# Optimization experiments

Hardware: AMD Instinct MI355X
Metric: run time of the kernel (lower is better)

The kernel has to match this reference:

```python
import jax, jax.numpy as jnp
import numpy as np

N_NODES = 100000
N_EDGES = 800000
EPS = 1e-5


def _mean_agg(h, src, dst):
    # DGL SAGEConv 'mean': average of in-neighbor features per dst node.
    msg = jnp.take(h, src, axis=0)                      # [E, D] gather
    summed = jax.ops.segment_sum(msg, dst, num_segments=N_NODES)
    deg = jax.ops.segment_sum(jnp.ones((src.shape[0],), h.dtype), dst,
                              num_segments=N_NODES)
    return summed / jnp.maximum(deg, 1.0)[:, None]


def _sage(h, src, dst, ws, wn, b):
    # rst = fc_self(h) + fc_neigh(mean_neigh) + bias
    return h @ ws + _mean_agg(h, src, dst) @ wn + b


def _bn(x, g, b, m, v):
    return (x - m) * (g / jnp.sqrt(v + EPS)) + b


def setup_inputs() -> dict:
    key = jax.random.key(0)
    ks = jax.random.split(key, 16)
    s = 0.02
    inp = {
        "structural_features": jax.random.normal(ks[0], (N_NODES, 128), jnp.float32),
        "multimodal_features": jax.random.normal(ks[1], (N_NODES, 384), jnp.float32),
        "src": jax.random.randint(ks[2], (N_EDGES,), 0, N_NODES),
        "dst": jax.random.randint(ks[3], (N_EDGES,), 0, N_NODES),
        "enc_w": jax.random.normal(ks[4], (512, 128), jnp.float32) * s,
        "enc_b": jnp.zeros((128,), jnp.float32),
        "sage0_ws": jax.random.normal(ks[5], (128, 256), jnp.float32) * s,
        "sage0_wn": jax.random.normal(ks[6], (128, 256), jnp.float32) * s,
        "sage0_b": jnp.zeros((256,), jnp.float32),
        "bn0_g": jnp.ones((256,), jnp.float32),
        "bn0_b": jnp.zeros((256,), jnp.float32),
        "bn0_m": jnp.zeros((256,), jnp.float32),
        "bn0_v": jnp.ones((256,), jnp.float32),
        "sage1_ws": jax.random.normal(ks[7], (256, 128), jnp.float32) * s,
        "sage1_wn": jax.random.normal(ks[8], (256, 128), jnp.float32) * s,
        "sage1_b": jnp.zeros((128,), jnp.float32),
        "bn1_g": jnp.ones((128,), jnp.float32),
        "bn1_b": jnp.zeros((128,), jnp.float32),
        "bn1_m": jnp.zeros((128,), jnp.float32),
        "bn1_v": jnp.ones((128,), jnp.float32),
        "rel_w": jax.random.normal(ks[9], (256, 128), jnp.float32) * s,
        "rel_b": jnp.zeros((128,), jnp.float32),
        "cls_w1": jax.random.normal(ks[10], (128, 64), jnp.float32) * s,
        "cls_b1": jnp.zeros((64,), jnp.float32),
        "cls_w2": jax.random.normal(ks[11], (64, 32), jnp.float32) * s,
        "cls_b2": jnp.zeros((32,), jnp.float32),
    }
    return inp


def reference(structural_features, multimodal_features, src, dst,
              enc_w, enc_b,
              sage0_ws, sage0_wn, sage0_b, bn0_g, bn0_b, bn0_m, bn0_v,
              sage1_ws, sage1_wn, sage1_b, bn1_g, bn1_b, bn1_m, bn1_v,
              rel_w, rel_b, cls_w1, cls_b1, cls_w2, cls_b2):
    x = jnp.concatenate([structural_features, multimodal_features], axis=-1)
    h0 = jax.nn.relu(x @ enc_w + enc_b)                     # input_encoder (dropout=eval)
    h = jax.nn.relu(_bn(_sage(h0, src, dst, sage0_ws, sage0_wn, sage0_b),
                        bn0_g, bn0_b, bn0_m, bn0_v))
    h = jax.nn.relu(_bn(_sage(h, src, dst, sage1_ws, sage1_wn, sage1_b),
                        bn1_g, bn1_b, bn1_m, bn1_v))
    h_final = jnp.concatenate([h0, h], axis=1)              # [N, 256]
    h_final = jax.nn.relu(h_final @ rel_w + rel_b)          # relation_encoder
    out = jax.nn.relu(h_final @ cls_w1 + cls_b1) @ cls_w2 + cls_b2
    return out
```

## Files before the change

### kernel.cpp

```cpp
#include <hip/hip_runtime.h>
#include <math.h>


#define EPS 1e-5f

typedef __attribute__((ext_vector_type(8))) short bf16x8;
typedef __attribute__((ext_vector_type(4))) float f32x4;

__device__ inline unsigned short f2bf(float x) {
    unsigned u = __float_as_uint(x);
    u += 0x7fff + ((u >> 16) & 1);
    return (unsigned short)(u >> 16);
}
__device__ inline float bf2f(unsigned short h) {
    return __uint_as_float(((unsigned)h) << 16);
}
__device__ inline unsigned packbf(float x, float y) {
    return (unsigned)f2bf(x) | ((unsigned)f2bf(y) << 16);
}

__device__ inline void gload_lds16(const void* g, void* l) {
    __builtin_amdgcn_global_load_lds(
        (__attribute__((address_space(1))) void*)g,
        (__attribute__((address_space(3))) void*)l, 16, 0, 0);
}


__global__ void count_deg(const int* __restrict__ dst, int* __restrict__ deg, int e) {
    int i = blockIdx.x * 256 + threadIdx.x;
    if (i < e) atomicAdd(&deg[dst[i]], 1);
}

__global__ __launch_bounds__(1024)
void scan_block(const int* __restrict__ deg, int* __restrict__ rowptr,
                int* __restrict__ part, int n) {
    __shared__ int buf[1024];
    const int tid = threadIdx.x;
    const int i = blockIdx.x * 1024 + tid;
    const int v = (i < n) ? deg[i] : 0;
    buf[tid] = v;
    __syncthreads();
    #pragma unroll 1
    for (int off = 1; off < 1024; off <<= 1) {
        int t = (tid >= off) ? buf[tid - off] : 0;
        __syncthreads();
        buf[tid] += t;
        __syncthreads();
    }
    if (i < n) rowptr[i] = buf[tid] - v;
    if (tid == 1023) part[blockIdx.x] = buf[1023];
}

__global__ __launch_bounds__(1024)
void scan_part(int* __restrict__ part, int nb) {
    __shared__ int buf[1024];
    const int tid = threadIdx.x;
    const int v = (tid < nb) ? part[tid] : 0;
    buf[tid] = v;
    __syncthreads();
    #pragma unroll 1
    for (int off = 1; off < 1024; off <<= 1) {
        int t = (tid >= off) ? buf[tid - off] : 0;
        __syncthreads();
        buf[tid] += t;
        __syncthreads();
    }
    if (tid < nb) part[tid] = buf[tid] - v;
    if (tid == 1023) part[nb] = buf[1023];
}

__global__ void scan_add(const int* __restrict__ part, int* __restrict__ rowptr,
                         int* __restrict__ cursor, int n, int nb) {
    int i = blockIdx.x * 256 + threadIdx.x;
    if (i < n) {
        int v = rowptr[i] + part[i >> 10];
        rowptr[i] = v;
        cursor[i] = v;
    }
    if (i == 0) rowptr[n] = part[nb];
}

__global__ void fill_edges(const int* __restrict__ src, const int* __restrict__ dst,
                           int* __restrict__ cursor, int* __restrict__ eidx, int e) {
    int i = blockIdx.x * 256 + threadIdx.x;
    if (i < e) {
        int pos = atomicAdd(&cursor[dst[i]], 1);
        eidx[pos] = src[i];
    }
}


__global__ __launch_bounds__(256)
void prep_all(const float* __restrict__ enc_w, const float* __restrict__ s0_ws,
              const float* __restrict__ s0_wn, const float* __restrict__ s1_ws,
              const float* __restrict__ s1_wn, const float* __restrict__ rel_w,
              const float* __restrict__ cw1, const float* __restrict__ cw2,
              short* wt_enc_h, short* wt_enc_l, short* wt_s0_h, short* wt_s0_l,
              short* wt_st_h, short* wt_st_l, short* wt_rel_h, short* wt_rel_l,
              short* wt_c1_h, short* wt_c1_l, short* wt_c2_h, short* wt_c2_l) {
    int e = blockIdx.x * 256 + threadIdx.x;
    const float* W; short* hi; short* lo; int Nd, ldt, koff;
    if (e < 65536)       { W = enc_w; hi = wt_enc_h; lo = wt_enc_l; Nd = 128; ldt = 512; koff = 0; }
    else if (e < 98304)  { e -= 65536;  W = s0_ws; hi = wt_s0_h; lo = wt_s0_l; Nd = 256; ldt = 256; koff = 0; }
    else if (e < 131072) { e -= 98304;  W = s0_wn; hi = wt_s0_h; lo = wt_s0_l; Nd = 256; ldt = 256; koff = 128; }
    else if (e < 163840) { e -= 131072; W = s1_ws; hi = wt_st_h; lo = wt_st_l; Nd = 128; ldt = 256; koff = 0; }
    else if (e < 196608) { e -= 163840; W = s1_wn; hi = wt_st_h + 32768; lo = wt_st_l + 32768; Nd = 128; ldt = 256; koff = 0; }
    else if (e < 229376) { e -= 196608; W = rel_w; hi = wt_rel_h; lo = wt_rel_l; Nd = 128; ldt = 256; koff = 0; }
    else if (e < 237568) { e -= 229376; W = cw1; hi = wt_c1_h; lo = wt_c1_l; Nd = 64; ldt = 128; koff = 0; }
    else if (e < 239616) { e -= 237568; W = cw2; hi = wt_c2_h; lo = wt_c2_l; Nd = 32; ldt = 64; koff = 0; }
    else return;
    const int k = e / Nd, n = e - k * Nd;
    const float x = W[e];
    const unsigned short h = f2bf(x);
    const unsigned short l = f2bf(x - bf2f(h));
    const size_t o = (size_t)n * ldt + koff + k;
    hi[o] = (short)h;
    lo[o] = (short)l;
}


__global__ __launch_bounds__(256)
void agg_mean_bb(const short* __restrict__ featb,
                 const int* __restrict__ rowptr, const int* __restrict__ eidx,
                 short* __restrict__ outb, int n) {
    const int node = blockIdx.x * 4 + (threadIdx.x >> 6);
    if (node >= n) return;
    const int lane = threadIdx.x & 63;
    const int g = lane >> 4, j = lane & 15;
    const int beg = rowptr[node], end = rowptr[node + 1];
    float s[8];
    #pragma unroll
    for (int i = 0; i < 8; ++i) s[i] = 0.f;
    for (int e = beg + g; e < end; e += 8) {
        const int e1 = e + 4;
        const bool has2 = e1 < end;
        const int i0 = eidx[e];
        const int i1 = has2 ? eidx[e1] : i0;
        const uint4 v0 = *(const uint4*)(featb + (size_t)i0 * 128 + j * 8);
        const uint4 v1 = *(const uint4*)(featb + (size_t)i1 * 128 + j * 8);
        __builtin_amdgcn_sched_barrier(0);
        s[0] += __uint_as_float(v0.x << 16); s[1] += __uint_as_float(v0.x & 0xffff0000u);
        s[2] += __uint_as_float(v0.y << 16); s[3] += __uint_as_float(v0.y & 0xffff0000u);
        s[4] += __uint_as_float(v0.z << 16); s[5] += __uint_as_float(v0.z & 0xffff0000u);
        s[6] += __uint_as_float(v0.w << 16); s[7] += __uint_as_float(v0.w & 0xffff0000u);
        if (has2) {
            s[0] += __uint_as_float(v1.x << 16); s[1] += __uint_as_float(v1.x & 0xffff0000u);
            s[2] += __uint_as_float(v1.y << 16); s[3] += __uint_as_float(v1.y & 0xffff0000u);
            s[4] += __uint_as_float(v1.z << 16); s[5] += __uint_as_float(v1.z & 0xffff0000u);
            s[6] += __uint_as_float(v1.w << 16); s[7] += __uint_as_float(v1.w & 0xffff0000u);
        }
    }
    #pragma unroll
    for (int i = 0; i < 8; ++i) {
        s[i] += __shfl_xor(s[i], 32);
        s[i] += __shfl_xor(s[i], 16);
    }
    if (g == 0) {
        const float inv = 1.0f / fmaxf((float)(end - beg), 1.0f);
        uint4 o;
        o.x = packbf(s[0] * inv, s[1] * inv);
        o.y = packbf(s[2] * inv, s[3] * inv);
        o.z = packbf(s[4] * inv, s[5] * inv);
        o.w = packbf(s[6] * inv, s[7] * inv);
        *(uint4*)(outb + (size_t)node * 128 + j * 8) = o;
    }
}

__global__ __launch_bounds__(256)
void agg_combine_bb(const short* __restrict__ featb,
                    const int* __restrict__ rowptr, const int* __restrict__ eidx,
                    const float* __restrict__ s1,
                    const float* __restrict__ bias,
                    const float* __restrict__ bng, const float* __restrict__ bnb,
                    const float* __restrict__ bnm, const float* __restrict__ bnv,
                    short* __restrict__ outb, int n) {
    const int node = blockIdx.x * 4 + (threadIdx.x >> 6);
    if (node >= n) return;
    const int lane = threadIdx.x & 63;
    const int g = lane >> 4, j = lane & 15;
    const int beg = rowptr[node], end = rowptr[node + 1];
    float s[8];
    #pragma unroll
    for (int i = 0; i < 8; ++i) s[i] = 0.f;
    for (int e = beg + g; e < end; e += 8) {
        const int e1 = e + 4;
        const bool has2 = e1 < end;
        const int i0 = eidx[e];
        const int i1 = has2 ? eidx[e1] : i0;
        const uint4 v0 = *(const uint4*)(featb + (size_t)i0 * 128 + j * 8);
        const uint4 v1 = *(const uint4*)(featb + (size_t)i1 * 128 + j * 8);
        __builtin_amdgcn_sched_barrier(0);
        s[0] += __uint_as_float(v0.x << 16); s[1] += __uint_as_float(v0.x & 0xffff0000u);
        s[2] += __uint_as_float(v0.y << 16); s[3] += __uint_as_float(v0.y & 0xffff0000u);
        s[4] += __uint_as_float(v0.z << 16); s[5] += __uint_as_float(v0.z & 0xffff0000u);
        s[6] += __uint_as_float(v0.w << 16); s[7] += __uint_as_float(v0.w & 0xffff0000u);
        if (has2) {
            s[0] += __uint_as_float(v1.x << 16); s[1] += __uint_as_float(v1.x & 0xffff0000u);
            s[2] += __uint_as_float(v1.y << 16); s[3] += __uint_as_float(v1.y & 0xffff0000u);
            s[4] += __uint_as_float(v1.z << 16); s[5] += __uint_as_float(v1.z & 0xffff0000u);
            s[6] += __uint_as_float(v1.w << 16); s[7] += __uint_as_float(v1.w & 0xffff0000u);
        }
    }
    #pragma unroll
    for (int i = 0; i < 8; ++i) {
        s[i] += __shfl_xor(s[i], 32);
        s[i] += __shfl_xor(s[i], 16);
    }
    if (g == 0) {
        const float inv = 1.0f / fmaxf((float)(end - beg), 1.0f);
        const int c0 = j * 8;
        const float4 a0 = *(const float4*)(s1 + (size_t)node * 128 + c0);
        const float4 a1 = *(const float4*)(s1 + (size_t)node * 128 + c0 + 4);
        const float sf[8] = {a0.x, a0.y, a0.z, a0.w, a1.x, a1.y, a1.z, a1.w};
        float r[8];
        #pragma unroll
        for (int i = 0; i < 8; ++i) {
            const int c = c0 + i;
            float v = sf[i] + s[i] * inv + bias[c];
            v = (v - bnm[c]) * (bng[c] / sqrtf(bnv[c] + EPS)) + bnb[c];
            r[i] = fmaxf(v, 0.f);
        }
        uint4 o;
        o.x = packbf(r[0], r[1]); o.y = packbf(r[2], r[3]);
        o.z = packbf(r[4], r[5]); o.w = packbf(r[6], r[7]);
        *(uint4*)(outb + (size_t)node * 128 + j * 8) = o;
    }
}

template<int NT, int K1, int K2>
__global__ __launch_bounds__(256)
void gemm_dp(const short* __restrict__ A1, int lda1,
             const short* __restrict__ A2, int lda2,
             const short* __restrict__ Wt_hi, const short* __restrict__ Wt_lo,
             const float* __restrict__ bias,
             const float* __restrict__ bng, const float* __restrict__ bnb,
             const float* __restrict__ bnm, const float* __restrict__ bnv,
             int relu,
             float* __restrict__ Cf, int fpN, int ldc,
             short* __restrict__ Cb, int bfcol0, int ldcb,
             int M) {
    constexpr int K   = K1 + K2;
    constexpr int NBK = K / 64;
    constexpr int NTW = NT / 2;
    static_assert(K % 64 == 0, "K multiple of 64");
    static_assert(NT % 2 == 0, "NT even");
    static_assert(K2 == 0 || K1 % 64 == 0, "concat boundary on BK");
    constexpr int ASZ = 128 * 64;
    constexpr int BSZ = 2 * NT * 16 * 64;
    constexpr int BUF = ASZ + BSZ;
    __shared__ short lds[2 * BUF];

    const int tid  = threadIdx.x;
    const int lane = tid & 63;
    const int wv   = tid >> 6;
    const int wm   = wv >> 1;
    const int wn   = wv & 1;
    const int bm   = blockIdx.y * 128;
    const int col0 = blockIdx.x * (NT * 16);
    const int lrow = lane & 15;
    const int quad = lane >> 4;

    const int su = (tid & 7) ^ ((tid >> 3) & 7);
    const short* gsA1[4];
    const short* gsA2[4];
    #pragma unroll
    for (int jj = 0; jj < 4; ++jj) {
        const int rg = min(bm + jj * 32 + (tid >> 3), M - 1);
        gsA1[jj] = A1 + (size_t)rg * lda1 + su * 8;
        if constexpr (K2 > 0) gsA2[jj] = A2 + (size_t)rg * lda2 + su * 8;
        else gsA2[jj] = nullptr;
    }
    const short* gsB[NT];
    #pragma unroll
    for (int jj = 0; jj < NT; ++jj) {
        const int colIdx = jj * 32 + (tid >> 3);
        const bool ishi = colIdx < NT * 16;
        const int cp = ishi ? colIdx : colIdx - NT * 16;
        gsB[jj] = (ishi ? Wt_hi : Wt_lo) + (size_t)(col0 + cp) * K + su * 8;
    }

    auto stage = [&](int b, int c) {
        const int k = c * 64;
        #pragma unroll
        for (int jj = 0; jj < 4; ++jj) {
            const short* p;
            if constexpr (K2 > 0)
                p = (k < K1) ? (gsA1[jj] + k) : (gsA2[jj] + (k - K1));
            else
                p = gsA1[jj] + k;
            gload_lds16(p, &lds[b * BUF + (jj * 256 + tid) * 8]);
        }
        #pragma unroll
        for (int jj = 0; jj < NT; ++jj)
            gload_lds16(gsB[jj] + k, &lds[b * BUF + ASZ + (jj * 256 + tid) * 8]);
    };

    int aoff[4][2];
    #pragma unroll
    for (int m = 0; m < 4; ++m)
        #pragma unroll
        for (int kk = 0; kk < 2; ++kk)
            aoff[m][kk] = (wm * 64 + m * 16 + lrow) * 64 +
                          (((kk * 4 + quad) ^ (lrow & 7)) * 8);
    int boff[NTW][2];
    #pragma unroll
    for (int nt = 0; nt < NTW; ++nt)
        #pragma unroll
        for (int kk = 0; kk < 2; ++kk)
            boff[nt][kk] = (wn * NTW * 16 + nt * 16 + lrow) * 64 +
                           (((kk * 4 + quad) ^ (lrow & 7)) * 8);

    f32x4 acc[4][NTW];
    #pragma unroll
    for (int m = 0; m < 4; ++m)
        #pragma unroll
        for (int nt = 0; nt < NTW; ++nt)
            acc[m][nt] = (f32x4){0.f, 0.f, 0.f, 0.f};

    stage(0, 0);

    for (int c = 0; c < NBK; ++c) {
        const int b = c & 1;
        if (c + 1 < NBK) {
            stage(b ^ 1, c + 1);
            if constexpr (NT == 4) asm volatile("s_waitcnt vmcnt(8)" ::: "memory");
            else                   asm volatile("s_waitcnt vmcnt(6)" ::: "memory");
        } else {
            asm volatile("s_waitcnt vmcnt(0)" ::: "memory");
        }
        __builtin_amdgcn_s_barrier();

        const short* La = &lds[b * BUF];
        const short* Lb = &lds[b * BUF + ASZ];
        #pragma unroll
        for (int kk = 0; kk < 2; ++kk) {
            bf16x8 a[4];
            #pragma unroll
            for (int m = 0; m < 4; ++m)
                a[m] = *(const bf16x8*)(La + aoff[m][kk]);
            #pragma unroll
            for (int nt = 0; nt < NTW; ++nt) {
                const bf16x8 vbh = *(const bf16x8*)(Lb + boff[nt][kk]);
                const bf16x8 vbl = *(const bf16x8*)(Lb + boff[nt][kk] + NT * 16 * 64);
                #pragma unroll
                for (int m = 0; m < 4; ++m) {
                    acc[m][nt] = __builtin_amdgcn_mfma_f32_16x16x32_bf16(a[m], vbh, acc[m][nt], 0, 0, 0);
                    acc[m][nt] = __builtin_amdgcn_mfma_f32_16x16x32_bf16(a[m], vbl, acc[m][nt], 0, 0, 0);
                }
            }
        }
        asm volatile("" ::: "memory");
        __builtin_amdgcn_s_barrier();
    }

    constexpr int EW = NT * 16 + 4;
    float* ep = (float*)lds;

    #pragma unroll
    for (int nt = 0; nt < NTW; ++nt) {
        const int lcol = wn * NTW * 16 + nt * 16 + lrow;
        const int gcol = col0 + lcol;
        const float bsc = bias ? bias[gcol] : 0.f;
        float gg = 1.f, bb = 0.f, mm = 0.f;
        if (bng) { gg = bng[gcol] / sqrtf(bnv[gcol] + EPS); bb = bnb[gcol]; mm = bnm[gcol]; }
        #pragma unroll
        for (int m = 0; m < 4; ++m) {
            #pragma unroll
            for (int r = 0; r < 4; ++r) {
                float x = acc[m][nt][r] + bsc;
                if (bng) x = (x - mm) * gg + bb;
                if (relu) x = fmaxf(x, 0.f);
                ep[(wm * 64 + m * 16 + quad * 4 + r) * EW + lcol] = x;
            }
        }
    }
    __syncthreads();

    if (col0 < fpN) {
        for (int g = tid; g < 128 * NT * 4; g += 256) {
            const int row = g / (NT * 4), u = g - row * (NT * 4);
            const int grow = bm + row;
            if (grow < M)
                *(float4*)(Cf + (size_t)grow * ldc + col0 + u * 4) =
                    *(const float4*)(ep + row * EW + u * 4);
        }
    } else {
        for (int g = tid; g < 128 * NT * 2; g += 256) {
            const int row = g / (NT * 2), u = g - row * (NT * 2);
            const int grow = bm + row;
            const float4 f0 = *(const float4*)(ep + row * EW + u * 8);
            const float4 f1 = *(const float4*)(ep + row * EW + u * 8 + 4);
            uint4 o;
            o.x = packbf(f0.x, f0.y); o.y = packbf(f0.z, f0.w);
            o.z = packbf(f1.x, f1.y); o.w = packbf(f1.z, f1.w);
            if (grow < M)
                *(uint4*)(Cb + (size_t)grow * ldcb + (col0 - bfcol0) + u * 8) = o;
        }
    }
}

__global__ __launch_bounds__(256)
void gemm_enc(const float* __restrict__ A1f,
              const float* __restrict__ A2f,
              const short* __restrict__ Wt_hi, const short* __restrict__ Wt_lo,
              const float* __restrict__ bias,
              short* __restrict__ Cb, int ldcb, int M) {
    constexpr int NT = 4, NTW = 2, K = 512, NBK = 8;
    constexpr int ASZ = 128 * 64;
    constexpr int BSZ = 2 * NT * 16 * 64;
    constexpr int BUF = ASZ + BSZ;
    __shared__ short lds[2 * BUF];

    const int tid  = threadIdx.x;
    const int lane = tid & 63;
    const int wv   = tid >> 6;
    const int wm   = wv >> 1;
    const int wn   = wv & 1;
    const int bm   = blockIdx.y * 128;
    const int col0 = blockIdx.x * (NT * 16);
    const int lrow = lane & 15;
    const int quad = lane >> 4;

    const int su = (tid & 7) ^ ((tid >> 3) & 7);
    const float* gsA1[4];
    const float* gsA2[4];
    #pragma unroll
    for (int jj = 0; jj < 4; ++jj) {
        const int rg = min(bm + jj * 32 + (tid >> 3), M - 1);
        gsA1[jj] = A1f + (size_t)rg * 128 + su * 8;
        gsA2[jj] = A2f + (size_t)rg * 384 + su * 8;
    }
    const short* gsB[NT];
    #pragma unroll
    for (int jj = 0; jj < NT; ++jj) {
        const int colIdx = jj * 32 + (tid >> 3);
        const bool ishi = colIdx < NT * 16;
        const int cp = ishi ? colIdx : colIdx - NT * 16;
        gsB[jj] = (ishi ? Wt_hi : Wt_lo) + (size_t)(col0 + cp) * K + su * 8;
    }
    auto stageB = [&](int b, int c) {
        const int k = c * 64;
        #pragma unroll
        for (int jj = 0; jj < NT; ++jj)
            gload_lds16(gsB[jj] + k, &lds[b * BUF + ASZ + (jj * 256 + tid) * 8]);
    };

    int aoff[4][2], boff[NTW][2];
    #pragma unroll
    for (int m = 0; m < 4; ++m)
        #pragma unroll
        for (int kk = 0; kk < 2; ++kk)
            aoff[m][kk] = (wm * 64 + m * 16 + lrow) * 64 +
                          (((kk * 4 + quad) ^ (lrow & 7)) * 8);
    #pragma unroll
    for (int nt = 0; nt < NTW; ++nt)
        #pragma unroll
        for (int kk = 0; kk < 2; ++kk)
            boff[nt][kk] = (wn * NTW * 16 + nt * 16 + lrow) * 64 +
                           (((kk * 4 + quad) ^ (lrow & 7)) * 8);

    f32x4 acc[4][NTW];
    #pragma unroll
    for (int m = 0; m < 4; ++m)
        #pragma unroll
        for (int nt = 0; nt < NTW; ++nt)
            acc[m][nt] = (f32x4){0.f, 0.f, 0.f, 0.f};

    float4 awin[8];

    #pragma unroll
    for (int jj = 0; jj < 4; ++jj) {
        awin[jj * 2 + 0] = *(const float4*)(gsA1[jj]);
        awin[jj * 2 + 1] = *(const float4*)(gsA1[jj] + 4);
    }
    stageB(0, 0);
    #pragma unroll
    for (int jj = 0; jj < 4; ++jj) {
        const float4 w0 = awin[jj * 2 + 0], w1 = awin[jj * 2 + 1];
        uint4 o;
        o.x = packbf(w0.x, w0.y); o.y = packbf(w0.z, w0.w);
        o.z = packbf(w1.x, w1.y); o.w = packbf(w1.z, w1.w);
        *((uint4*)&lds[(jj * 256 + tid) * 8]) = o;
    }
    asm volatile("s_waitcnt vmcnt(0)" ::: "memory");
    __builtin_amdgcn_s_barrier();

    #pragma unroll
    for (int c = 0; c < NBK; ++c) {
        const int cur = c & 1, nxt = cur ^ 1;
        if (c + 1 < NBK) {
            const int k1 = (c + 1) * 64;
            #pragma unroll
            for (int jj = 0; jj < 4; ++jj) {
                const float* p = (k1 < 128) ? (gsA1[jj] + k1)
                                            : (gsA2[jj] + (k1 - 128));
                awin[jj * 2 + 0] = *(const float4*)p;
                awin[jj * 2 + 1] = *(const float4*)(p + 4);
            }
            stageB(nxt, c + 1);
            __builtin_amdgcn_sched_barrier(0);
        }

        const short* La = &lds[cur * BUF];
        const short* Lb = &lds[cur * BUF + ASZ];
        #pragma unroll
        for (int kk = 0; kk < 2; ++kk) {
            bf16x8 a[4];
            #pragma unroll
            for (int m = 0; m < 4; ++m)
                a[m] = *(const bf16x8*)(La + aoff[m][kk]);
            #pragma unroll
            for (int nt = 0; nt < NTW; ++nt) {
                const bf16x8 vbh = *(const bf16x8*)(Lb + boff[nt][kk]);
                const bf16x8 vbl = *(const bf16x8*)(Lb + boff[nt][kk] + NT * 16 * 64);
                #pragma unroll
                for (int m = 0; m < 4; ++m) {
                    acc[m][nt] = __builtin_amdgcn_mfma_f32_16x16x32_bf16(a[m], vbh, acc[m][nt], 0, 0, 0);
                    acc[m][nt] = __builtin_amdgcn_mfma_f32_16x16x32_bf16(a[m], vbl, acc[m][nt], 0, 0, 0);
                }
            }
        }

        if (c + 1 < NBK) {
            #pragma unroll
            for (int jj = 0; jj < 4; ++jj) {
                const float4 w0 = awin[jj * 2 + 0], w1 = awin[jj * 2 + 1];
                uint4 o;
                o.x = packbf(w0.x, w0.y); o.y = packbf(w0.z, w0.w);
                o.z = packbf(w1.x, w1.y); o.w = packbf(w1.z, w1.w);
                *((uint4*)&lds[nxt * BUF + (jj * 256 + tid) * 8]) = o;
            }
            asm volatile("s_waitcnt vmcnt(0)" ::: "memory");
            __builtin_amdgcn_s_barrier();
        }
    }
    __builtin_amdgcn_s_barrier();

    constexpr int EW = NT * 16 + 4;
    float* ep = (float*)lds;
    #pragma unroll
    for (int nt = 0; nt < NTW; ++nt) {
        const int lcol = wn * NTW * 16 + nt * 16 + lrow;
        const float bsc = bias[col0 + lcol];
        #pragma unroll
        for (int m = 0; m < 4; ++m)
            #pragma unroll
            for (int r = 0; r < 4; ++r)
                ep[(wm * 64 + m * 16 + quad * 4 + r) * EW + lcol] =
                    fmaxf(acc[m][nt][r] + bsc, 0.f);
    }
    __syncthreads();
    for (int g = tid; g < 128 * NT * 2; g += 256) {
        const int row = g / (NT * 2), u = g - row * (NT * 2);
        const int grow = bm + row;
        const float4 f0 = *(const float4*)(ep + row * EW + u * 8);
        const float4 f1 = *(const float4*)(ep + row * EW + u * 8 + 4);
        uint4 o;
        o.x = packbf(f0.x, f0.y); o.y = packbf(f0.z, f0.w);
        o.z = packbf(f1.x, f1.y); o.w = packbf(f1.z, f1.w);
        if (grow < M)
            *(uint4*)(Cb + (size_t)grow * ldcb + col0 + u * 8) = o;
    }
}

__global__ __launch_bounds__(256)
void gemm_cls(const short* __restrict__ A1,
              const short* __restrict__ W1h, const short* __restrict__ W1l,
              const float* __restrict__ cb1,
              const short* __restrict__ W2h, const short* __restrict__ W2l,
              const float* __restrict__ cb2,
              float* __restrict__ out, int M) {
    constexpr int NT = 4, NTW = 2, NBK = 2, K = 128;
    constexpr int ASZ = 128 * 64, BSZ = 2 * NT * 16 * 64, BUF = ASZ + BSZ;
    __shared__ short lds[2 * BUF];

    const int tid  = threadIdx.x;
    const int lane = tid & 63;
    const int wv   = tid >> 6;
    const int wm   = wv >> 1;
    const int wn   = wv & 1;
    const int bm   = blockIdx.x * 128;
    const int lrow = lane & 15;
    const int quad = lane >> 4;

    const int su = (tid & 7) ^ ((tid >> 3) & 7);
    const short* gsA[4];
    #pragma unroll
    for (int jj = 0; jj < 4; ++jj) {
        const int rg = min(bm + jj * 32 + (tid >> 3), M - 1);
        gsA[jj] = A1 + (size_t)rg * 128 + su * 8;
    }
    const short* gsB[NT];
    #pragma unroll
    for (int jj = 0; jj < NT; ++jj) {
        const int colIdx = jj * 32 + (tid >> 3);
        const bool ishi = colIdx < NT * 16;
        const int cp = ishi ? colIdx : colIdx - NT * 16;
        gsB[jj] = (ishi ? W1h : W1l) + (size_t)cp * K + su * 8;
    }
    auto stage = [&](int b, int c) {
        const int k = c * 64;
        #pragma unroll
        for (int jj = 0; jj < 4; ++jj)
            gload_lds16(gsA[jj] + k, &lds[b * BUF + (jj * 256 + tid) * 8]);
        #pragma unroll
        for (int jj = 0; jj < NT; ++jj)
            gload_lds16(gsB[jj] + k, &lds[b * BUF + ASZ + (jj * 256 + tid) * 8]);
    };

    int aoff[4][2], boff[NTW][2];
    #pragma unroll
    for (int m = 0; m < 4; ++m)
        #pragma unroll
        for (int kk = 0; kk < 2; ++kk)
            aoff[m][kk] = (wm * 64 + m * 16 + lrow) * 64 +
                          (((kk * 4 + quad) ^ (lrow & 7)) * 8);
    #pragma unroll
    for (int nt = 0; nt < NTW; ++nt)
        #pragma unroll
        for (int kk = 0; kk < 2; ++kk)
            boff[nt][kk] = (wn * NTW * 16 + nt * 16 + lrow) * 64 +
                           (((kk * 4 + quad) ^ (lrow & 7)) * 8);

    f32x4 acc[4][NTW];
    #pragma unroll
    for (int m = 0; m < 4; ++m)
        #pragma unroll
        for (int nt = 0; nt < NTW; ++nt)
            acc[m][nt] = (f32x4){0.f, 0.f, 0.f, 0.f};

    stage(0, 0);
    for (int c = 0; c < NBK; ++c) {
        const int b = c & 1;
        if (c + 1 < NBK) {
            stage(b ^ 1, c + 1);
            asm volatile("s_waitcnt vmcnt(8)" ::: "memory");
        } else {
            asm volatile("s_waitcnt vmcnt(0)" ::: "memory");
        }
        __builtin_amdgcn_s_barrier();
        const short* La = &lds[b * BUF];
        const short* Lb = &lds[b * BUF + ASZ];
        #pragma unroll
        for (int kk = 0; kk < 2; ++kk) {
            bf16x8 a[4];
            #pragma unroll
            for (int m = 0; m < 4; ++m)
                a[m] = *(const bf16x8*)(La + aoff[m][kk]);
            #pragma unroll
            for (int nt = 0; nt < NTW; ++nt) {
                const bf16x8 vbh = *(const bf16x8*)(Lb + boff[nt][kk]);
                const bf16x8 vbl = *(const bf16x8*)(Lb + boff[nt][kk] + NT * 16 * 64);
                #pragma unroll
                for (int m = 0; m < 4; ++m) {
                    acc[m][nt] = __builtin_amdgcn_mfma_f32_16x16x32_bf16(a[m], vbh, acc[m][nt], 0, 0, 0);
                    acc[m][nt] = __builtin_amdgcn_mfma_f32_16x16x32_bf16(a[m], vbl, acc[m][nt], 0, 0, 0);
                }
            }
        }
        asm volatile("" ::: "memory");
        __builtin_amdgcn_s_barrier();
    }

    constexpr int EW = 68;
    float* ep = (float*)lds;
    #pragma unroll
    for (int nt = 0; nt < NTW; ++nt) {
        const int lcol = wn * NTW * 16 + nt * 16 + lrow;
        const float bsc = cb1[lcol];
        #pragma unroll
        for (int m = 0; m < 4; ++m)
            #pragma unroll
            for (int r = 0; r < 4; ++r)
                ep[(wm * 64 + m * 16 + quad * 4 + r) * EW + lcol] =
                    fmaxf(acc[m][nt][r] + bsc, 0.f);
    }
    __syncthreads();

    const short* pB2h = W2h + (size_t)(wn * 16 + lrow) * 64 + quad * 8;
    const short* pB2l = W2l + (size_t)(wn * 16 + lrow) * 64 + quad * 8;
    f32x4 acc2[4];
    #pragma unroll
    for (int m = 0; m < 4; ++m) acc2[m] = (f32x4){0.f, 0.f, 0.f, 0.f};
    #pragma unroll
    for (int kk = 0; kk < 2; ++kk) {
        const bf16x8 bh = *(const bf16x8*)(pB2h + kk * 32);
        const bf16x8 bl = *(const bf16x8*)(pB2l + kk * 32);
        #pragma unroll
        for (int m = 0; m < 4; ++m) {
            const float* pe = ep + (wm * 64 + m * 16 + lrow) * EW + kk * 32 + quad * 8;
            const float4 e0 = *(const float4*)pe;
            const float4 e1 = *(const float4*)(pe + 4);
            bf16x8 a;
            a[0] = (short)f2bf(e0.x); a[1] = (short)f2bf(e0.y);
            a[2] = (short)f2bf(e0.z); a[3] = (short)f2bf(e0.w);
            a[4] = (short)f2bf(e1.x); a[5] = (short)f2bf(e1.y);
            a[6] = (short)f2bf(e1.z); a[7] = (short)f2bf(e1.w);
            acc2[m] = __builtin_amdgcn_mfma_f32_16x16x32_bf16(a, bh, acc2[m], 0, 0, 0);
            acc2[m] = __builtin_amdgcn_mfma_f32_16x16x32_bf16(a, bl, acc2[m], 0, 0, 0);
        }
    }

    constexpr int EW2 = 36;
    float* ep2 = (float*)lds + 128 * EW;
    {
        const int lcol = wn * 16 + lrow;
        const float bsc = cb2[lcol];
        #pragma unroll
        for (int m = 0; m < 4; ++m)
            #pragma unroll
            for (int r = 0; r < 4; ++r)
                ep2[(wm * 64 + m * 16 + quad * 4 + r) * EW2 + lcol] =
                    acc2[m][r] + bsc;
    }
    __syncthreads();
    #pragma unroll
    for (int j = 0; j < 4; ++j) {
        const int g = tid + j * 256;
        const int row = g >> 3, u = g & 7;
        const int grow = bm + row;
        if (grow < M)
            *(float4*)(out + (size_t)grow * 32 + u * 4) =
                *(const float4*)(ep2 + row * EW2 + u * 4);
    }
}


extern "C" void kernel_launch(void* const* d_in, const int* in_sizes, int n_in,
                              void* d_out, int out_size, void* d_ws, size_t ws_size,
                              hipStream_t stream) {
    const float* sf    = (const float*)d_in[0];
    const float* mf    = (const float*)d_in[1];
    const int*   src   = (const int*)d_in[2];
    const int*   dst   = (const int*)d_in[3];
    const float* enc_w = (const float*)d_in[4];
    const float* enc_b = (const float*)d_in[5];
    const float* s0_ws = (const float*)d_in[6];
    const float* s0_wn = (const float*)d_in[7];
    const float* s0_b  = (const float*)d_in[8];
    const float* bn0_g = (const float*)d_in[9];
    const float* bn0_b = (const float*)d_in[10];
    const float* bn0_m = (const float*)d_in[11];
    const float* bn0_v = (const float*)d_in[12];
    const float* s1_ws = (const float*)d_in[13];
    const float* s1_wn = (const float*)d_in[14];
    const float* s1_b  = (const float*)d_in[15];
    const float* bn1_g = (const float*)d_in[16];
    const float* bn1_b = (const float*)d_in[17];
    const float* bn1_m = (const float*)d_in[18];
    const float* bn1_v = (const float*)d_in[19];
    const float* rel_w = (const float*)d_in[20];
    const float* rel_b = (const float*)d_in[21];
    const float* cw1   = (const float*)d_in[22];
    const float* cb1   = (const float*)d_in[23];
    const float* cw2   = (const float*)d_in[24];
    const float* cb2   = (const float*)d_in[25];
    float* out = (float*)d_out;

    const int nn = in_sizes[0] / 128;
    const int ne = in_sizes[2];
    const int nb = (nn + 1023) / 1024;

    short* h0b   = (short*)d_ws;
    short* xb    = h0b + (size_t)nn * 128;
    float* st    = (float*)xb;
    short* h1b   = (short*)(st + (size_t)nn * 128);
    short* agg0b = xb + (size_t)nn * 512;
    short* t1b   = agg0b + (size_t)nn * 128;
    short* h2b   = t1b + (size_t)nn * 128;
    short* rb    = t1b;
    int* deg    = (int*)(h2b + (size_t)nn * 128);
    int* rowptr = deg + nn;
    int* cursor = rowptr + nn + 1;
    int* part   = cursor + nn;
    int* eidx   = part + nb + 1;
    short* wts = (short*)(eidx + ne);
    short* wt_enc_h = wts;                 short* wt_enc_l = wt_enc_h + 65536;
    short* wt_s0_h  = wt_enc_l + 65536;    short* wt_s0_l  = wt_s0_h  + 65536;
    short* wt_st_h  = wt_s0_l  + 65536;    short* wt_st_l  = wt_st_h  + 65536;
    short* wt_rel_h = wt_st_l  + 65536;    short* wt_rel_l = wt_rel_h + 32768;
    short* wt_c1_h  = wt_rel_l + 32768;    short* wt_c1_l  = wt_c1_h  + 8192;
    short* wt_c2_h  = wt_c1_l  + 8192;     short* wt_c2_l  = wt_c2_h  + 2048;

    const dim3 blk(256);
    const int gM = (nn + 127) / 128;

    hipMemsetAsync(deg, 0, (size_t)nn * 4, stream);
    count_deg <<<dim3((ne + 255) / 256), blk, 0, stream>>>(dst, deg, ne);
    scan_block<<<dim3(nb), dim3(1024), 0, stream>>>(deg, rowptr, part, nn);
    scan_part <<<dim3(1),  dim3(1024), 0, stream>>>(part, nb);
    scan_add  <<<dim3((nn + 255) / 256), blk, 0, stream>>>(part, rowptr, cursor, nn, nb);
    fill_edges<<<dim3((ne + 255) / 256), blk, 0, stream>>>(src, dst, cursor, eidx, ne);

    prep_all<<<dim3(936), blk, 0, stream>>>(
        enc_w, s0_ws, s0_wn, s1_ws, s1_wn, rel_w, cw1, cw2,
        wt_enc_h, wt_enc_l, wt_s0_h, wt_s0_l, wt_st_h, wt_st_l,
        wt_rel_h, wt_rel_l, wt_c1_h, wt_c1_l, wt_c2_h, wt_c2_l);

    gemm_enc<<<dim3(2, gM), blk, 0, stream>>>(
        sf, mf, wt_enc_h, wt_enc_l, enc_b, h0b, 128, nn);

    agg_mean_bb<<<dim3((nn + 3) / 4), blk, 0, stream>>>(
        h0b, rowptr, eidx, agg0b, nn);

    gemm_dp<4, 128, 128><<<dim3(4, gM), blk, 0, stream>>>(
        h0b, 128, agg0b, 128, wt_s0_h, wt_s0_l, s0_b,
        bn0_g, bn0_b, bn0_m, bn0_v, 1,
        nullptr, 0, 0, h1b, 0, 256, nn);

    gemm_dp<4, 256, 0><<<dim3(4, gM), blk, 0, stream>>>(
        h1b, 256, nullptr, 0, wt_st_h, wt_st_l, nullptr,
        nullptr, nullptr, nullptr, nullptr, 0,
        st, 128, 128, t1b, 128, 128, nn);

    agg_combine_bb<<<dim3((nn + 3) / 4), blk, 0, stream>>>(
        t1b, rowptr, eidx, st, s1_b,
        bn1_g, bn1_b, bn1_m, bn1_v, h2b, nn);

    gemm_dp<4, 128, 128><<<dim3(2, gM), blk, 0, stream>>>(
        h0b, 128, h2b, 128, wt_rel_h, wt_rel_l, rel_b,
        nullptr, nullptr, nullptr, nullptr, 1,
        nullptr, 0, 0, rb, 0, 128, nn);

    gemm_cls<<<dim3(gM), blk, 0, stream>>>(
        rb, wt_c1_h, wt_c1_l, cb1, wt_c2_h, wt_c2_l, cb2, out, nn);
}
```

Before: 661.3 us.

## Fuse relation encoder GEMM into classifier kernel to skip intermediate round trip

Merges the relation-encoder GEMM (concat of h0 and h2, K=256, N=128) with the two classifier layers into a single kernel. Each block now computes the full 128-column relation output and keeps it in LDS as the input to cls layer 1, with cls weights read straight from global memory. This removes one launch and the bf16 write and re-read of the intermediate relation tensor. In exchange, grid parallelism drops from 2*gM to gM blocks and each block's register and LDS footprint grows, which may lower occupancy.

```diff
diff --git a/kernel.cpp b/kernel.cpp
--- a/kernel.cpp
+++ b/kernel.cpp
@@ -564,14 +564,19 @@
 }
 
 __global__ __launch_bounds__(256)
-void gemm_cls(const short* __restrict__ A1,
-              const short* __restrict__ W1h, const short* __restrict__ W1l,
-              const float* __restrict__ cb1,
-              const short* __restrict__ W2h, const short* __restrict__ W2l,
-              const float* __restrict__ cb2,
-              float* __restrict__ out, int M) {
-    constexpr int NT = 4, NTW = 2, NBK = 2, K = 128;
-    constexpr int ASZ = 128 * 64, BSZ = 2 * NT * 16 * 64, BUF = ASZ + BSZ;
+void gemm_relcls(const short* __restrict__ A1,
+                 const short* __restrict__ A2,
+                 const short* __restrict__ Wh, const short* __restrict__ Wl,
+                 const float* __restrict__ rel_b,
+                 const short* __restrict__ W1h, const short* __restrict__ W1l,
+                 const float* __restrict__ cb1,
+                 const short* __restrict__ W2h, const short* __restrict__ W2l,
+                 const float* __restrict__ cb2,
+                 float* __restrict__ out, int M) {
+    constexpr int NT = 8, NTW = 4, NBK = 4, K = 256;
+    constexpr int ASZ = 128 * 64;
+    constexpr int BSZ = 2 * NT * 16 * 64;
+    constexpr int BUF = ASZ + BSZ;
     __shared__ short lds[2 * BUF];
 
     const int tid  = threadIdx.x;
@@ -584,25 +589,29 @@
     const int quad = lane >> 4;
 
     const int su = (tid & 7) ^ ((tid >> 3) & 7);
-    const short* gsA[4];
+    const short* gsA1[4];
+    const short* gsA2[4];
     #pragma unroll
     for (int jj = 0; jj < 4; ++jj) {
         const int rg = min(bm + jj * 32 + (tid >> 3), M - 1);
-        gsA[jj] = A1 + (size_t)rg * 128 + su * 8;
+        gsA1[jj] = A1 + (size_t)rg * 128 + su * 8;
+        gsA2[jj] = A2 + (size_t)rg * 128 + su * 8;
     }
     const short* gsB[NT];
     #pragma unroll
     for (int jj = 0; jj < NT; ++jj) {
         const int colIdx = jj * 32 + (tid >> 3);
-        const bool ishi = colIdx < NT * 16;
-        const int cp = ishi ? colIdx : colIdx - NT * 16;
-        gsB[jj] = (ishi ? W1h : W1l) + (size_t)cp * K + su * 8;
+        const bool ishi = colIdx < 128;
+        const int cp = ishi ? colIdx : colIdx - 128;
+        gsB[jj] = (ishi ? Wh : Wl) + (size_t)cp * K + su * 8;
     }
     auto stage = [&](int b, int c) {
         const int k = c * 64;
         #pragma unroll
-        for (int jj = 0; jj < 4; ++jj)
-            gload_lds16(gsA[jj] + k, &lds[b * BUF + (jj * 256 + tid) * 8]);
+        for (int jj = 0; jj < 4; ++jj) {
+            const short* p = (k < 128) ? (gsA1[jj] + k) : (gsA2[jj] + (k - 128));
+            gload_lds16(p, &lds[b * BUF + (jj * 256 + tid) * 8]);
+        }
         #pragma unroll
         for (int jj = 0; jj < NT; ++jj)
             gload_lds16(gsB[jj] + k, &lds[b * BUF + ASZ + (jj * 256 + tid) * 8]);
@@ -619,7 +628,7 @@
     for (int nt = 0; nt < NTW; ++nt)
         #pragma unroll
         for (int kk = 0; kk < 2; ++kk)
-            boff[nt][kk] = (wn * NTW * 16 + nt * 16 + lrow) * 64 +
+            boff[nt][kk] = (wn * 64 + nt * 16 + lrow) * 64 +
                            (((kk * 4 + quad) ^ (lrow & 7)) * 8);
 
     f32x4 acc[4][NTW];
@@ -634,11 +643,12 @@
         const int b = c & 1;
         if (c + 1 < NBK) {
             stage(b ^ 1, c + 1);
-            asm volatile("s_waitcnt vmcnt(8)" ::: "memory");
+            asm volatile("s_waitcnt vmcnt(12)" ::: "memory");
         } else {
             asm volatile("s_waitcnt vmcnt(0)" ::: "memory");
         }
         __builtin_amdgcn_s_barrier();
+
         const short* La = &lds[b * BUF];
         const short* Lb = &lds[b * BUF + ASZ];
         #pragma unroll
@@ -650,7 +660,7 @@
             #pragma unroll
             for (int nt = 0; nt < NTW; ++nt) {
                 const bf16x8 vbh = *(const bf16x8*)(Lb + boff[nt][kk]);
-                const bf16x8 vbl = *(const bf16x8*)(Lb + boff[nt][kk] + NT * 16 * 64);
+                const bf16x8 vbl = *(const bf16x8*)(Lb + boff[nt][kk] + 128 * 64);
                 #pragma unroll
                 for (int m = 0; m < 4; ++m) {
                     acc[m][nt] = __builtin_amdgcn_mfma_f32_16x16x32_bf16(a[m], vbh, acc[m][nt], 0, 0, 0);
@@ -662,33 +672,39 @@
         __builtin_amdgcn_s_barrier();
     }
 
-    constexpr int EW = 68;
-    float* ep = (float*)lds;
+    constexpr int EW1 = 132;
+    float* rt = (float*)lds;
     #pragma unroll
     for (int nt = 0; nt < NTW; ++nt) {
-        const int lcol = wn * NTW * 16 + nt * 16 + lrow;
-        const float bsc = cb1[lcol];
+        const int lcol = wn * 64 + nt * 16 + lrow;
+        const float bsc = rel_b[lcol];
         #pragma unroll
         for (int m = 0; m < 4; ++m)
             #pragma unroll
             for (int r = 0; r < 4; ++r)
-                ep[(wm * 64 + m * 16 + quad * 4 + r) * EW + lcol] =
+                rt[(wm * 64 + m * 16 + quad * 4 + r) * EW1 + lcol] =
                     fmaxf(acc[m][nt][r] + bsc, 0.f);
     }
     __syncthreads();
 
-    const short* pB2h = W2h + (size_t)(wn * 16 + lrow) * 64 + quad * 8;
-    const short* pB2l = W2l + (size_t)(wn * 16 + lrow) * 64 + quad * 8;
-    f32x4 acc2[4];
-    #pragma unroll
-    for (int m = 0; m < 4; ++m) acc2[m] = (f32x4){0.f, 0.f, 0.f, 0.f};
-    #pragma unroll
-    for (int kk = 0; kk < 2; ++kk) {
-        const bf16x8 bh = *(const bf16x8*)(pB2h + kk * 32);
-        const bf16x8 bl = *(const bf16x8*)(pB2l + kk * 32);
+    f32x4 acc2[4][2];
+    #pragma unroll
+    for (int m = 0; m < 4; ++m)
+        #pragma unroll
+        for (int nt = 0; nt < 2; ++nt)
+            acc2[m][nt] = (f32x4){0.f, 0.f, 0.f, 0.f};
+    #pragma unroll
+    for (int kk = 0; kk < 4; ++kk) {
+        bf16x8 b2h[2], b2l[2];
+        #pragma unroll
+        for (int nt = 0; nt < 2; ++nt) {
+            const size_t cw = (size_t)(wn * 32 + nt * 16 + lrow) * 128 + kk * 32 + quad * 8;
+            b2h[nt] = *(const bf16x8*)(W1h + cw);
+            b2l[nt] = *(const bf16x8*)(W1l + cw);
+        }
         #pragma unroll
         for (int m = 0; m < 4; ++m) {
-            const float* pe = ep + (wm * 64 + m * 16 + lrow) * EW + kk * 32 + quad * 8;
+            const float* pe = rt + (wm * 64 + m * 16 + lrow) * EW1 + kk * 32 + quad * 8;
             const float4 e0 = *(const float4*)pe;
             const float4 e1 = *(const float4*)(pe + 4);
             bf16x8 a;
@@ -696,13 +712,56 @@
             a[2] = (short)f2bf(e0.z); a[3] = (short)f2bf(e0.w);
             a[4] = (short)f2bf(e1.x); a[5] = (short)f2bf(e1.y);
             a[6] = (short)f2bf(e1.z); a[7] = (short)f2bf(e1.w);
-            acc2[m] = __builtin_amdgcn_mfma_f32_16x16x32_bf16(a, bh, acc2[m], 0, 0, 0);
-            acc2[m] = __builtin_amdgcn_mfma_f32_16x16x32_bf16(a, bl, acc2[m], 0, 0, 0);
-        }
-    }
-
-    constexpr int EW2 = 36;
-    float* ep2 = (float*)lds + 128 * EW;
+            #pragma unroll
+            for (int nt = 0; nt < 2; ++nt) {
+                acc2[m][nt] = __builtin_amdgcn_mfma_f32_16x16x32_bf16(a, b2h[nt], acc2[m][nt], 0, 0, 0);
+                acc2[m][nt] = __builtin_amdgcn_mfma_f32_16x16x32_bf16(a, b2l[nt], acc2[m][nt], 0, 0, 0);
+            }
+        }
+    }
+    __syncthreads();
+
+    constexpr int EW2 = 68;
+    float* ep2 = (float*)lds;
+    #pragma unroll
+    for (int nt = 0; nt < 2; ++nt) {
+        const int lcol = wn * 32 + nt * 16 + lrow;
+        const float bsc = cb1[lcol];
+        #pragma unroll
+        for (int m = 0; m < 4; ++m)
+            #pragma unroll
+            for (int r = 0; r < 4; ++r)
+                ep2[(wm * 64 + m * 16 + quad * 4 + r) * EW2 + lcol] =
+                    fmaxf(acc2[m][nt][r] + bsc, 0.f);
+    }
+    __syncthreads();
+
+    const short* pB3h = W2h + (size_t)(wn * 16 + lrow) * 64 + quad * 8;
+    const short* pB3l = W2l + (size_t)(wn * 16 + lrow) * 64 + quad * 8;
+    f32x4 acc3[4];
+    #pragma unroll
+    for (int m = 0; m < 4; ++m) acc3[m] = (f32x4){0.f, 0.f, 0.f, 0.f};
+    #pragma unroll
+    for (int kk = 0; kk < 2; ++kk) {
+        const bf16x8 bh = *(const bf16x8*)(pB3h + kk * 32);
+        const bf16x8 bl = *(const bf16x8*)(pB3l + kk * 32);
+        #pragma unroll
+        for (int m = 0; m < 4; ++m) {
+            const float* pe = ep2 + (wm * 64 + m * 16 + lrow) * EW2 + kk * 32 + quad * 8;
+            const float4 e0 = *(const float4*)pe;
+            const float4 e1 = *(const float4*)(pe + 4);
+            bf16x8 a;
+            a[0] = (short)f2bf(e0.x); a[1] = (short)f2bf(e0.y);
+            a[2] = (short)f2bf(e0.z); a[3] = (short)f2bf(e0.w);
+            a[4] = (short)f2bf(e1.x); a[5] = (short)f2bf(e1.y);
+            a[6] = (short)f2bf(e1.z); a[7] = (short)f2bf(e1.w);
+            acc3[m] = __builtin_amdgcn_mfma_f32_16x16x32_bf16(a, bh, acc3[m], 0, 0, 0);
+            acc3[m] = __builtin_amdgcn_mfma_f32_16x16x32_bf16(a, bl, acc3[m], 0, 0, 0);
+        }
+    }
+
+    constexpr int EW3 = 36;
+    float* ep3 = (float*)lds + 128 * EW2;
     {
         const int lcol = wn * 16 + lrow;
         const float bsc = cb2[lcol];
@@ -710,8 +769,8 @@
         for (int m = 0; m < 4; ++m)
             #pragma unroll
             for (int r = 0; r < 4; ++r)
-                ep2[(wm * 64 + m * 16 + quad * 4 + r) * EW2 + lcol] =
-                    acc2[m][r] + bsc;
+                ep3[(wm * 64 + m * 16 + quad * 4 + r) * EW3 + lcol] =
+                    acc3[m][r] + bsc;
     }
     __syncthreads();
     #pragma unroll
@@ -721,7 +780,7 @@
         const int grow = bm + row;
         if (grow < M)
             *(float4*)(out + (size_t)grow * 32 + u * 4) =
-                *(const float4*)(ep2 + row * EW2 + u * 4);
+                *(const float4*)(ep3 + row * EW3 + u * 4);
     }
 }
 
@@ -768,7 +827,6 @@
     short* agg0b = xb + (size_t)nn * 512;
     short* t1b   = agg0b + (size_t)nn * 128;
     short* h2b   = t1b + (size_t)nn * 128;
-    short* rb    = t1b;
     int* deg    = (int*)(h2b + (size_t)nn * 128);
     int* rowptr = deg + nn;
     int* cursor = rowptr + nn + 1;
@@ -817,11 +875,7 @@
         t1b, rowptr, eidx, st, s1_b,
         bn1_g, bn1_b, bn1_m, bn1_v, h2b, nn);
 
-    gemm_dp<4, 128, 128><<<dim3(2, gM), blk, 0, stream>>>(
-        h0b, 128, h2b, 128, wt_rel_h, wt_rel_l, rel_b,
-        nullptr, nullptr, nullptr, nullptr, 1,
-        nullptr, 0, 0, rb, 0, 128, nn);
-
-    gemm_cls<<<dim3(gM), blk, 0, stream>>>(
-        rb, wt_c1_h, wt_c1_l, cb1, wt_c2_h, wt_c2_l, cb2, out, nn);
-}
+    gemm_relcls<<<dim3(gM), blk, 0, stream>>>(
+        h0b, h2b, wt_rel_h, wt_rel_l, rel_b,
+        wt_c1_h, wt_c1_l, cb1, wt_c2_h, wt_c2_l, cb2, out, nn);
+}
```

Result: no change. 659.4 us (-0.3%).
